# Optimization experiments

Hardware: AMD Instinct MI355X
Metric: run time of the kernel (lower is better)

Reference implementation:

```python
import jax, jax.numpy as jnp
import numpy as np

B, N, S, D, H, ITERS = 32, 4096, 24, 256, 4, 3
DH = D // H
SCALE = DH ** -0.5
EPS = 1e-8
LN_EPS = 1e-5


def _ln(x, g, b):
    m = x.mean(-1, keepdims=True)
    v = ((x - m) ** 2).mean(-1, keepdims=True)
    return (x - m) * jax.lax.rsqrt(v + LN_EPS) * g + b


def setup_inputs() -> dict:
    key = jax.random.key(0)
    ks = jax.random.split(key, 20)
    xav = lambda k, fi, fo: jax.random.uniform(k, (fi, fo), jnp.float32, -1.0, 1.0) * np.sqrt(6.0 / (fi + fo))
    u = lambda k, shp, fan: jax.random.uniform(k, shp, jnp.float32, -1.0, 1.0) / np.sqrt(fan)
    return {
        "extracted_features": jax.random.normal(ks[0], (B, N, D), jnp.float32),
        "conditioning": jax.random.normal(ks[1], (B, S, D), jnp.float32),
        "pos_ln_g": jnp.ones((D,), jnp.float32),
        "pos_ln_b": jnp.zeros((D,), jnp.float32),
        "pos_w1": xav(ks[2], D, D),
        "pos_b1": jnp.zeros((D,), jnp.float32),
        "pos_w2": xav(ks[3], D, D),
        "pos_b2": jnp.zeros((D,), jnp.float32),
        "in_ln_g": jnp.ones((D,), jnp.float32),
        "in_ln_b": jnp.zeros((D,), jnp.float32),
        "slot_ln_g": jnp.ones((D,), jnp.float32),
        "slot_ln_b": jnp.zeros((D,), jnp.float32),
        "Wq": u(ks[4], (D, D), D),
        "Wk": u(ks[5], (D, D), D),
        "Wv": u(ks[6], (D, D), D),
        "gru_wi": u(ks[7], (D, 3 * D), D),  # x @ gru_wi, torch weight_ih.T
        "gru_wh": u(ks[8], (D, 3 * D), D),
        "gru_bi": u(ks[9], (3 * D,), D),
        "gru_bh": u(ks[10], (3 * D,), D),
    }


def reference(extracted_features, conditioning, pos_ln_g, pos_ln_b, pos_w1, pos_b1,
              pos_w2, pos_b2, in_ln_g, in_ln_b, slot_ln_g, slot_ln_b,
              Wq, Wk, Wv, gru_wi, gru_wh, gru_bi, gru_bh):
    b, n, _ = extracted_features.shape
    s = conditioning.shape[1]
    # positional embedding MLP: LN -> Linear -> ReLU -> Linear
    feats = _ln(extracted_features, pos_ln_g, pos_ln_b)
    feats = jax.nn.relu(feats @ pos_w1 + pos_b1) @ pos_w2 + pos_b2
    # slot attention input norm + k/v projections
    inp = _ln(feats, in_ln_g, in_ln_b)
    k = (inp @ Wk).reshape(b, n, H, DH)
    v = (inp @ Wv).reshape(b, n, H, DH)

    slots = conditioning
    attn_before = None
    for _ in range(ITERS):
        slots_prev = slots
        sn = _ln(slots, slot_ln_g, slot_ln_b)
        q = (sn @ Wq).reshape(b, s, H, DH)
        dots = jnp.einsum('bihd,bjhd->bihj', q, k) * SCALE  # [b,s,H,n]
        # softmax over flattened (slot, head) axis per input token
        attn = jax.nn.softmax(dots.reshape(b, s * H, n), axis=1).reshape(b, s, H, n)
        attn_before = attn
        attn_r = (attn + EPS)
        attn_r = attn_r / attn_r.sum(-1, keepdims=True)
        updates = jnp.einsum('bjhd,bihj->bihd', v, attn_r).reshape(b * s, D)
        # GRUCell update
        h = slots_prev.reshape(b * s, D)
        gi = updates @ gru_wi + gru_bi
        gh = h @ gru_wh + gru_bh
        ir, iz, inn = jnp.split(gi, 3, axis=-1)
        hr, hz, hn = jnp.split(gh, 3, axis=-1)
        r = jax.nn.sigmoid(ir + hr)
        z = jax.nn.sigmoid(iz + hz)
        nn_ = jnp.tanh(inn + r * hn)
        slots = ((1.0 - z) * nn_ + z * h).reshape(b, s, D)

    return slots, attn_before.mean(axis=2)
```

## Files before the change

kernel.cpp:

```cpp
#include <hip/hip_runtime.h>
#include <hip/hip_bf16.h>
#include <stdint.h>

typedef __hip_bfloat16 bf16;
typedef __attribute__((ext_vector_type(8))) short short8;
typedef __attribute__((ext_vector_type(4))) float floatx4;

#define DEV __device__ __forceinline__

DEV float bf2f(bf16 v) { return __bfloat162float(v); }
DEV bf16 f2b(float f) { return __float2bfloat16(f); }
DEV unsigned short f2bu(float f) {
  bf16 h = __float2bfloat16(f);
  union { bf16 h; unsigned short u; } c; c.h = h; return c.u;
}


__global__ void detect_kernel(const unsigned short* probe, int* flag) {
  *flag = (probe[0] != 0) ? 1 : 0;
}

__global__ __launch_bounds__(256) void params_kernel(
    const void* s0, const void* s1, const void* s2, const void* s3, const void* s4,
    const void* s5, const void* s6, const void* s7, const void* s8, const void* s9,
    float* dst, const int* flagp)
{
  int idx = blockIdx.x * 256 + threadIdx.x;
  if (idx >= 3584) return;
  const void* srcs[10] = {s0, s1, s2, s3, s4, s5, s6, s7, s8, s9};
  int a, off;
  if (idx < 2048)      { a = idx >> 8; off = idx & 255; }
  else if (idx < 2816) { a = 8; off = idx - 2048; }
  else                 { a = 9; off = idx - 2816; }
  float v = (*flagp) ? bf2f(((const bf16*)srcs[a])[off]) : ((const float*)srcs[a])[off];
  dst[idx] = v;
}

__global__ __launch_bounds__(256) void transpose_convert_kernel(
    const void* src, bf16* dst, int R, int C, const int* flagp)
{
  int idx = blockIdx.x * 256 + threadIdx.x;
  if (idx >= R * C) return;
  int r = idx / C, c = idx - r * C;
  bf16 v = (*flagp) ? ((const bf16*)src)[idx] : f2b(((const float*)src)[idx]);
  dst[(size_t)c * R + r] = v;
}

template<bool OUT_BF16, bool RELU, bool HAS_BIAS>
__global__ __launch_bounds__(256) void gemm_kernel(
    const bf16* __restrict__ A, const bf16* __restrict__ Bt,
    const float* __restrict__ bias, void* __restrict__ C,
    int M, int N, int K)
{
  __shared__ short As[128 * 72];
  __shared__ short Bs[128 * 72];
  const int tid = threadIdx.x;
  const int lane = tid & 63;
  const int wave = tid >> 6;
  const int wr = wave >> 1, wc = wave & 1;
  const int m16 = lane & 15, quad = lane >> 4;
  const long m0 = (long)blockIdx.y * 128, n0 = (long)blockIdx.x * 128;

  floatx4 acc[4][4];
#pragma unroll
  for (int i = 0; i < 4; i++)
#pragma unroll
    for (int j = 0; j < 4; j++) acc[i][j] = {0.f, 0.f, 0.f, 0.f};

  const int srow = tid >> 3;
  const int scol = (tid & 7) * 8;

  for (int kb = 0; kb < K; kb += 64) {
#pragma unroll
    for (int p = 0; p < 4; p++) {
      int row = srow + p * 32;
      uint4 av = *(const uint4*)(A + (m0 + row) * (long)K + kb + scol);
      *(uint4*)(&As[row * 72 + scol]) = av;
      uint4 bv = *(const uint4*)(Bt + (n0 + row) * (long)K + kb + scol);
      *(uint4*)(&Bs[row * 72 + scol]) = bv;
    }
    __syncthreads();
#pragma unroll
    for (int ks = 0; ks < 2; ks++) {
      short8 af[4], bfr[4];
#pragma unroll
      for (int t = 0; t < 4; t++) {
        af[t]  = *(const short8*)(&As[(wr * 64 + t * 16 + m16) * 72 + ks * 32 + quad * 8]);
        bfr[t] = *(const short8*)(&Bs[(wc * 64 + t * 16 + m16) * 72 + ks * 32 + quad * 8]);
      }
#pragma unroll
      for (int mt = 0; mt < 4; mt++)
#pragma unroll
        for (int nt = 0; nt < 4; nt++)
          acc[mt][nt] = __builtin_amdgcn_mfma_f32_16x16x32_bf16(af[mt], bfr[nt], acc[mt][nt], 0, 0, 0);
    }
    __syncthreads();
  }

#pragma unroll
  for (int mt = 0; mt < 4; mt++) {
#pragma unroll
    for (int nt = 0; nt < 4; nt++) {
      long col = n0 + wc * 64 + nt * 16 + m16;
      float bb = HAS_BIAS ? bias[col] : 0.f;
#pragma unroll
      for (int r = 0; r < 4; r++) {
        long row = m0 + wr * 64 + mt * 16 + quad * 4 + r;
        float v = acc[mt][nt][r] + bb;
        if (RELU) v = fmaxf(v, 0.f);
        if (OUT_BF16) ((bf16*)C)[row * N + col] = f2b(v);
        else          ((float*)C)[row * N + col] = v;
      }
    }
  }
}

template<int MODE>
__global__ __launch_bounds__(256) void ln_kernel(
    const void* __restrict__ xin, const float* __restrict__ g, const float* __restrict__ bb,
    bf16* __restrict__ out, int rows, const int* flagp)
{
  int wave = threadIdx.x >> 6, lane = threadIdx.x & 63;
  long row = (long)blockIdx.x * 4 + wave;
  if (row >= rows) return;
  float v[4];
  bool f32in = (MODE == 1) || (MODE == 2 && *flagp == 0);
  if (f32in) {
    float4 f = *(const float4*)((const float*)xin + row * 256 + lane * 4);
    v[0] = f.x; v[1] = f.y; v[2] = f.z; v[3] = f.w;
  } else {
    uint2 u = *(const uint2*)((const bf16*)xin + row * 256 + lane * 4);
    v[0] = __uint_as_float((u.x & 0xffffu) << 16);
    v[1] = __uint_as_float(u.x & 0xffff0000u);
    v[2] = __uint_as_float((u.y & 0xffffu) << 16);
    v[3] = __uint_as_float(u.y & 0xffff0000u);
  }
  float s = v[0] + v[1] + v[2] + v[3];
  float sq = v[0] * v[0] + v[1] * v[1] + v[2] * v[2] + v[3] * v[3];
#pragma unroll
  for (int off = 32; off > 0; off >>= 1) {
    s  += __shfl_xor(s, off);
    sq += __shfl_xor(sq, off);
  }
  float m = s * (1.f / 256.f);
  float var = sq * (1.f / 256.f) - m * m;
  float rs = rsqrtf(var + 1e-5f);
  float4 gv = *(const float4*)(g + lane * 4);
  float4 bv = *(const float4*)(bb + lane * 4);
  union { unsigned short us[4]; uint2 u; } pk;
  pk.us[0] = f2bu((v[0] - m) * rs * gv.x + bv.x);
  pk.us[1] = f2bu((v[1] - m) * rs * gv.y + bv.y);
  pk.us[2] = f2bu((v[2] - m) * rs * gv.z + bv.z);
  pk.us[3] = f2bu((v[3] - m) * rs * gv.w + bv.w);
  *(uint2*)(out + row * 256 + lane * 4) = pk.u;
}

__global__ __launch_bounds__(256) void init_slots_kernel(
    const void* __restrict__ cond, float* __restrict__ sF, bf16* __restrict__ sB,
    const int* flagp)
{
  int idx = blockIdx.x * 256 + threadIdx.x;
  float v = (*flagp) ? bf2f(((const bf16*)cond)[idx]) : ((const float*)cond)[idx];
  sF[idx] = v;
  sB[idx] = f2b(v);
}

__global__ __launch_bounds__(256) void repack_q_kernel(
    const float* __restrict__ q, bf16* __restrict__ qp)
{
  int idx = blockIdx.x * 256 + threadIdx.x;
  int dh = idx & 63, m = (idx >> 6) & 31, h = (idx >> 11) & 3, b = idx >> 13;
  float val = 0.f;
  if (m < 24) val = q[((size_t)(b * 24 + m)) * 256 + h * 64 + dh] * 0.125f;
  qp[idx] = f2b(val);
}

template<bool LAST>
__global__ __launch_bounds__(256) void attn_iter_kernel(
    const bf16* __restrict__ qp, const bf16* __restrict__ kbuf,
    const bf16* __restrict__ vT, float* __restrict__ pupd,
    void* __restrict__ out, const int* flagp)
{
  const int js = blockIdx.x;
  const int b  = blockIdx.y;
  const int h  = threadIdx.x >> 6;
  const int lane = threadIdx.x & 63;
  const int m16 = lane & 15, quad = lane >> 4;
  const int j0 = js * 128;

  __shared__ unsigned short att[4 * 24 * 136];
  __shared__ float red1[4 * 132];
  __shared__ float red2[4 * 132];

  short8 qf[2][2];
  const bf16* qpb = qp + (size_t)(b * 4 + h) * 2048;
#pragma unroll
  for (int mt = 0; mt < 2; mt++)
#pragma unroll
    for (int ks = 0; ks < 2; ks++)
      qf[mt][ks] = *(const short8*)(qpb + (mt * 16 + m16) * 64 + ks * 32 + quad * 8);

  floatx4 dacc[2][8];
#pragma unroll
  for (int i = 0; i < 2; i++)
#pragma unroll
    for (int j = 0; j < 8; j++) dacc[i][j] = {0.f, 0.f, 0.f, 0.f};

  const bf16* kb = kbuf + ((size_t)b * 4096 + j0) * 256 + h * 64;
#pragma unroll
  for (int ks = 0; ks < 2; ks++)
#pragma unroll
    for (int nt = 0; nt < 8; nt++) {
      short8 bfr = *(const short8*)(kb + (size_t)(nt * 16 + m16) * 256 + ks * 32 + quad * 8);
      dacc[0][nt] = __builtin_amdgcn_mfma_f32_16x16x32_bf16(qf[0][ks], bfr, dacc[0][nt], 0, 0, 0);
      dacc[1][nt] = __builtin_amdgcn_mfma_f32_16x16x32_bf16(qf[1][ks], bfr, dacc[1][nt], 0, 0, 0);
    }

  const bool mt1_valid = (quad < 2);

  float cmax[8];
#pragma unroll
  for (int nt = 0; nt < 8; nt++) {
    float m = fmaxf(fmaxf(dacc[0][nt][0], dacc[0][nt][1]), fmaxf(dacc[0][nt][2], dacc[0][nt][3]));
    if (mt1_valid)
      m = fmaxf(m, fmaxf(fmaxf(dacc[1][nt][0], dacc[1][nt][1]), fmaxf(dacc[1][nt][2], dacc[1][nt][3])));
    m = fmaxf(m, __shfl_xor(m, 16));
    m = fmaxf(m, __shfl_xor(m, 32));
    cmax[nt] = m;
  }
  if (quad == 0) {
#pragma unroll
    for (int nt = 0; nt < 8; nt++) red1[h * 132 + nt * 16 + m16] = cmax[nt];
  }
  __syncthreads();

  float csum[8];
#pragma unroll
  for (int nt = 0; nt < 8; nt++) {
    int c = nt * 16 + m16;
    float g = fmaxf(fmaxf(red1[c], red1[132 + c]), fmaxf(red1[264 + c], red1[396 + c]));
    float s = 0.f;
#pragma unroll
    for (int r = 0; r < 4; r++) {
      float e = __expf(dacc[0][nt][r] - g);
      dacc[0][nt][r] = e; s += e;
    }
#pragma unroll
    for (int r = 0; r < 4; r++) {
      float e = mt1_valid ? __expf(dacc[1][nt][r] - g) : 0.f;
      dacc[1][nt][r] = e; s += e;
    }
    s += __shfl_xor(s, 16);
    s += __shfl_xor(s, 32);
    csum[nt] = s;
  }
  if (quad == 0) {
#pragma unroll
    for (int nt = 0; nt < 8; nt++) red2[h * 132 + nt * 16 + m16] = csum[nt];
  }
  __syncthreads();

  float wsum[2][4] = {{0.f, 0.f, 0.f, 0.f}, {0.f, 0.f, 0.f, 0.f}};
#pragma unroll
  for (int nt = 0; nt < 8; nt++) {
    int c = nt * 16 + m16;
    float inv = 1.f / (red2[c] + red2[132 + c] + red2[264 + c] + red2[396 + c]);
#pragma unroll
    for (int r = 0; r < 4; r++) {
      float a = dacc[0][nt][r] * inv + 1e-8f;
      int row = quad * 4 + r;
      att[h * 3264 + row * 136 + c] = f2bu(a);
      wsum[0][r] += a;
    }
    if (mt1_valid) {
#pragma unroll
      for (int r = 0; r < 4; r++) {
        float a = dacc[1][nt][r] * inv + 1e-8f;
        int row = 16 + quad * 4 + r;
        att[h * 3264 + row * 136 + c] = f2bu(a);
        wsum[1][r] += a;
      }
    }
  }
#pragma unroll
  for (int mt = 0; mt < 2; mt++)
#pragma unroll
    for (int r = 0; r < 4; r++) {
      float w = wsum[mt][r];
      w += __shfl_xor(w, 1); w += __shfl_xor(w, 2);
      w += __shfl_xor(w, 4); w += __shfl_xor(w, 8);
      wsum[mt][r] = w;
    }
  float* dst = pupd + ((size_t)(b * 4 + h) * 32 + js) * 1920;
  if (m16 == 0) {
#pragma unroll
    for (int mt = 0; mt < 2; mt++)
#pragma unroll
      for (int r = 0; r < 4; r++) {
        int row = mt * 16 + quad * 4 + r;
        if (row < 24) dst[row * 80 + 64] = wsum[mt][r];
      }
  }
  __syncthreads();

  floatx4 uacc[2][4];
#pragma unroll
  for (int i = 0; i < 2; i++)
#pragma unroll
    for (int j = 0; j < 4; j++) uacc[i][j] = {0.f, 0.f, 0.f, 0.f};
  int arow1 = 16 + m16; if (arow1 > 23) arow1 = 23;
  const bf16* vb0 = vT + (size_t)b * 4096 + j0;
#pragma unroll
  for (int ks = 0; ks < 4; ks++) {
    short8 a0 = *(const short8*)(&att[h * 3264 + m16 * 136 + ks * 32 + quad * 8]);
    short8 a1 = *(const short8*)(&att[h * 3264 + arow1 * 136 + ks * 32 + quad * 8]);
#pragma unroll
    for (int nt = 0; nt < 4; nt++) {
      short8 bfr = *(const short8*)(vb0 + (size_t)(h * 64 + nt * 16 + m16) * 131072 + ks * 32 + quad * 8);
      uacc[0][nt] = __builtin_amdgcn_mfma_f32_16x16x32_bf16(a0, bfr, uacc[0][nt], 0, 0, 0);
      uacc[1][nt] = __builtin_amdgcn_mfma_f32_16x16x32_bf16(a1, bfr, uacc[1][nt], 0, 0, 0);
    }
  }
#pragma unroll
  for (int mt = 0; mt < 2; mt++)
#pragma unroll
    for (int nt = 0; nt < 4; nt++)
#pragma unroll
      for (int r = 0; r < 4; r++) {
        int row = mt * 16 + quad * 4 + r;
        if (row < 24) dst[row * 80 + nt * 16 + m16] = uacc[mt][nt][r];
      }

  if (LAST) {
    int c = threadIdx.x & 127;
    int half = threadIdx.x >> 7;
#pragma unroll
    for (int i0 = 0; i0 < 12; i0++) {
      int i = half * 12 + i0;
      float s = bf2f(__ushort_as_bfloat16(att[i * 136 + c]))
              + bf2f(__ushort_as_bfloat16(att[3264 + i * 136 + c]))
              + bf2f(__ushort_as_bfloat16(att[6528 + i * 136 + c]))
              + bf2f(__ushort_as_bfloat16(att[9792 + i * 136 + c]));
      size_t oidx = ((size_t)(b * 24 + i)) * 4096 + j0 + c;
      if (*flagp) ((bf16*)out)[196608 + oidx] = f2b(0.25f * s);
      else        ((float*)out)[196608 + oidx] = 0.25f * s;
    }
  }
}

__global__ __launch_bounds__(256) void upd_final_kernel(
    const float* __restrict__ pupd, bf16* __restrict__ updB)
{
  int bh = blockIdx.x; int b = bh >> 2, h = bh & 3;
  int idx = blockIdx.y * 256 + threadIdx.x;
  int i = idx >> 6, d = idx & 63;
  const float* base = pupd + (size_t)bh * 32 * 1920 + i * 80;
  float v = 0.f, w = 0.f;
#pragma unroll
  for (int p = 0; p < 32; p++) {
    v += base[p * 1920 + d];
    w += base[p * 1920 + 64];
  }
  updB[((size_t)(b * 24 + i)) * 256 + h * 64 + d] = f2b(v / w);
}

__global__ __launch_bounds__(256) void gru_gate_kernel(
    const float* __restrict__ gi, const float* __restrict__ gh,
    float* __restrict__ sF, bf16* __restrict__ sB)
{
  int row = blockIdx.x, d = threadIdx.x;
  size_t o = (size_t)row * 768;
  float ir = gi[o + d], iz = gi[o + 256 + d], inn = gi[o + 512 + d];
  float hr = gh[o + d], hz = gh[o + 256 + d], hn = gh[o + 512 + d];
  float hv = sF[(size_t)row * 256 + d];
  float r = 1.f / (1.f + __expf(-(ir + hr)));
  float z = 1.f / (1.f + __expf(-(iz + hz)));
  float nn = tanhf(inn + r * hn);
  float sv = (1.f - z) * nn + z * hv;
  sF[(size_t)row * 256 + d] = sv;
  sB[(size_t)row * 256 + d] = f2b(sv);
}

__global__ __launch_bounds__(256) void out_slots_kernel(
    const float* __restrict__ sF, void* __restrict__ out, const int* flagp)
{
  int idx = blockIdx.x * 256 + threadIdx.x;
  float v = sF[idx];
  if (*flagp) ((bf16*)out)[idx] = f2b(v);
  else        ((float*)out)[idx] = v;
}

static constexpr size_t SZ_BIG   = (size_t)32 * 4096 * 256 * 2;
static constexpr size_t OFF_BUF1 = 0;
static constexpr size_t OFF_BUF2 = OFF_BUF1 + SZ_BIG;
static constexpr size_t OFF_K    = OFF_BUF2 + SZ_BIG;
static constexpr size_t OFF_V    = OFF_K + SZ_BIG;
static constexpr size_t OFF_Q    = OFF_V + SZ_BIG;
static constexpr size_t OFF_QP   = OFF_Q + (size_t)768 * 256 * 4;
static constexpr size_t OFF_SNB  = OFF_QP + (size_t)32 * 4 * 32 * 64 * 2;
static constexpr size_t OFF_SF   = OFF_SNB + (size_t)768 * 256 * 2;
static constexpr size_t OFF_SB   = OFF_SF + (size_t)768 * 256 * 4;
static constexpr size_t OFF_UPD  = OFF_SB + (size_t)768 * 256 * 2;
static constexpr size_t OFF_GI   = OFF_UPD + (size_t)768 * 256 * 2;
static constexpr size_t OFF_GH   = OFF_GI + (size_t)768 * 768 * 4;
static constexpr size_t OFF_PUPD = OFF_GH + (size_t)768 * 768 * 4;
static constexpr size_t OFF_W1T  = OFF_PUPD + (size_t)128 * 32 * 1920 * 4;
static constexpr size_t OFF_W2T  = OFF_W1T + (size_t)256 * 256 * 2;
static constexpr size_t OFF_WQT  = OFF_W2T + (size_t)256 * 256 * 2;
static constexpr size_t OFF_WKT  = OFF_WQT + (size_t)256 * 256 * 2;
static constexpr size_t OFF_WVT  = OFF_WKT + (size_t)256 * 256 * 2;
static constexpr size_t OFF_GWIT = OFF_WVT + (size_t)256 * 256 * 2;
static constexpr size_t OFF_GWHT = OFF_GWIT + (size_t)256 * 768 * 2;
static constexpr size_t OFF_PAR  = OFF_GWHT + (size_t)256 * 768 * 2;
static constexpr size_t OFF_FLAG = OFF_PAR + (size_t)3584 * 4;
static constexpr size_t WS_NEED  = OFF_FLAG + 256;

extern "C" void kernel_launch(void* const* d_in, const int* in_sizes, int n_in,
                              void* d_out, int out_size, void* d_ws, size_t ws_size,
                              hipStream_t stream) {
  (void)in_sizes; (void)n_in; (void)out_size;
  if (ws_size < WS_NEED) return;

  const void* x         = d_in[0];
  const void* cond      = d_in[1];
  const void* pos_ln_g  = d_in[2];
  const void* pos_ln_b  = d_in[3];
  const void* pos_w1    = d_in[4];
  const void* pos_b1    = d_in[5];
  const void* pos_w2    = d_in[6];
  const void* pos_b2    = d_in[7];
  const void* in_ln_g   = d_in[8];
  const void* in_ln_b   = d_in[9];
  const void* slot_ln_g = d_in[10];
  const void* slot_ln_b = d_in[11];
  const void* Wq        = d_in[12];
  const void* Wk        = d_in[13];
  const void* Wv        = d_in[14];
  const void* gru_wi    = d_in[15];
  const void* gru_wh    = d_in[16];
  const void* gru_bi    = d_in[17];
  const void* gru_bh    = d_in[18];

  char* ws = (char*)d_ws;
  bf16*  buf1  = (bf16*)(ws + OFF_BUF1);
  bf16*  buf2  = (bf16*)(ws + OFF_BUF2);
  bf16*  kbuf  = (bf16*)(ws + OFF_K);
  bf16*  vT    = (bf16*)(ws + OFF_V);
  float* qbuf  = (float*)(ws + OFF_Q);
  bf16*  qp    = (bf16*)(ws + OFF_QP);
  bf16*  snb   = (bf16*)(ws + OFF_SNB);
  float* sF    = (float*)(ws + OFF_SF);
  bf16*  sB    = (bf16*)(ws + OFF_SB);
  bf16*  updB  = (bf16*)(ws + OFF_UPD);
  float* gi    = (float*)(ws + OFF_GI);
  float* gh    = (float*)(ws + OFF_GH);
  float* pupd  = (float*)(ws + OFF_PUPD);
  bf16*  w1t   = (bf16*)(ws + OFF_W1T);
  bf16*  w2t   = (bf16*)(ws + OFF_W2T);
  bf16*  wqt   = (bf16*)(ws + OFF_WQT);
  bf16*  wkt   = (bf16*)(ws + OFF_WKT);
  bf16*  wvt   = (bf16*)(ws + OFF_WVT);
  bf16*  gwit  = (bf16*)(ws + OFF_GWIT);
  bf16*  gwht  = (bf16*)(ws + OFF_GWHT);
  float* par   = (float*)(ws + OFF_PAR);
  int*   flagp = (int*)(ws + OFF_FLAG);

  detect_kernel<<<1, 1, 0, stream>>>((const unsigned short*)pos_ln_g, flagp);
  params_kernel<<<14, 256, 0, stream>>>(pos_ln_g, pos_ln_b, pos_b1, pos_b2,
                                        in_ln_g, in_ln_b, slot_ln_g, slot_ln_b,
                                        gru_bi, gru_bh, par, flagp);
  transpose_convert_kernel<<<256, 256, 0, stream>>>(pos_w1, w1t, 256, 256, flagp);
  transpose_convert_kernel<<<256, 256, 0, stream>>>(pos_w2, w2t, 256, 256, flagp);
  transpose_convert_kernel<<<256, 256, 0, stream>>>(Wq, wqt, 256, 256, flagp);
  transpose_convert_kernel<<<256, 256, 0, stream>>>(Wk, wkt, 256, 256, flagp);
  transpose_convert_kernel<<<256, 256, 0, stream>>>(Wv, wvt, 256, 256, flagp);
  transpose_convert_kernel<<<768, 256, 0, stream>>>(gru_wi, gwit, 256, 768, flagp);
  transpose_convert_kernel<<<768, 256, 0, stream>>>(gru_wh, gwht, 256, 768, flagp);
  init_slots_kernel<<<768, 256, 0, stream>>>(cond, sF, sB, flagp);

  ln_kernel<2><<<32768, 256, 0, stream>>>(x, par + 0, par + 256, buf1, 131072, flagp);
  gemm_kernel<true, true, true><<<dim3(2, 1024), 256, 0, stream>>>(
      buf1, w1t, par + 512, buf2, 131072, 256, 256);
  gemm_kernel<true, false, true><<<dim3(2, 1024), 256, 0, stream>>>(
      buf2, w2t, par + 768, buf1, 131072, 256, 256);
  ln_kernel<0><<<32768, 256, 0, stream>>>(buf1, par + 1024, par + 1280, buf2, 131072, flagp);
  gemm_kernel<true, false, false><<<dim3(2, 1024), 256, 0, stream>>>(
      buf2, wkt, nullptr, kbuf, 131072, 256, 256);
  gemm_kernel<true, false, false><<<dim3(1024, 2), 256, 0, stream>>>(
      wvt, buf2, nullptr, vT, 256, 131072, 256);

  for (int it = 0; it < 3; it++) {
    ln_kernel<1><<<192, 256, 0, stream>>>(sF, par + 1536, par + 1792, snb, 768, flagp);
    gemm_kernel<false, false, false><<<dim3(2, 6), 256, 0, stream>>>(
        snb, wqt, nullptr, qbuf, 768, 256, 256);
    repack_q_kernel<<<1024, 256, 0, stream>>>(qbuf, qp);
    if (it == 2)
      attn_iter_kernel<true><<<dim3(32, 32), 256, 0, stream>>>(qp, kbuf, vT, pupd, d_out, flagp);
    else
      attn_iter_kernel<false><<<dim3(32, 32), 256, 0, stream>>>(qp, kbuf, vT, pupd, d_out, flagp);
    upd_final_kernel<<<dim3(128, 6), 256, 0, stream>>>(pupd, updB);
    gemm_kernel<false, false, true><<<dim3(6, 6), 256, 0, stream>>>(
        updB, gwit, par + 2048, gi, 768, 768, 256);
    gemm_kernel<false, false, true><<<dim3(6, 6), 256, 0, stream>>>(
        sB, gwht, par + 2816, gh, 768, 768, 256);
    gru_gate_kernel<<<768, 256, 0, stream>>>(gi, gh, sF, sB);
  }

  out_slots_kernel<<<768, 256, 0, stream>>>(sF, d_out, flagp);
}
```

Measured before the change: 679.8 us.

## Fuse layernorms into GEMMs, merge weight prep and GRU GEMMs, widen attention tiles

```diff
diff --git a/kernel.cpp b/kernel.cpp
--- a/kernel.cpp
+++ b/kernel.cpp
@@ -14,52 +14,72 @@
   bf16 h = __float2bfloat16(f);
   union { bf16 h; unsigned short u; } c; c.h = h; return c.u;
 }
-
-
-__global__ void detect_kernel(const unsigned short* probe, int* flag) {
-  *flag = (probe[0] != 0) ? 1 : 0;
-}
+DEV bool is_bf16_in(const void* probe) { return ((const unsigned short*)probe)[0] != 0; }
+
 
 __global__ __launch_bounds__(256) void params_kernel(
     const void* s0, const void* s1, const void* s2, const void* s3, const void* s4,
     const void* s5, const void* s6, const void* s7, const void* s8, const void* s9,
-    float* dst, const int* flagp)
+    float* dst)
 {
   int idx = blockIdx.x * 256 + threadIdx.x;
   if (idx >= 3584) return;
+  bool bf = is_bf16_in(s0);
   const void* srcs[10] = {s0, s1, s2, s3, s4, s5, s6, s7, s8, s9};
   int a, off;
   if (idx < 2048)      { a = idx >> 8; off = idx & 255; }
   else if (idx < 2816) { a = 8; off = idx - 2048; }
   else                 { a = 9; off = idx - 2816; }
-  float v = (*flagp) ? bf2f(((const bf16*)srcs[a])[off]) : ((const float*)srcs[a])[off];
+  float v = bf ? bf2f(((const bf16*)srcs[a])[off]) : ((const float*)srcs[a])[off];
   dst[idx] = v;
 }
 
-__global__ __launch_bounds__(256) void transpose_convert_kernel(
-    const void* src, bf16* dst, int R, int C, const int* flagp)
+__global__ __launch_bounds__(256) void transpose_all_kernel(
+    const void* w1, const void* w2, const void* wq, const void* wk, const void* wv,
+    const void* gwi, const void* gwh,
+    bf16* d1, bf16* d2, bf16* dq, bf16* dk, bf16* dv, bf16* dgi, bf16* dgh,
+    const void* probe)
 {
   int idx = blockIdx.x * 256 + threadIdx.x;
-  if (idx >= R * C) return;
-  int r = idx / C, c = idx - r * C;
-  bf16 v = (*flagp) ? ((const bf16*)src)[idx] : f2b(((const float*)src)[idx]);
-  dst[(size_t)c * R + r] = v;
+  if (idx >= 720896) return;
+  bool bf = is_bf16_in(probe);
+  const void* src; bf16* dst; int C, off;
+  if (idx < 327680) {
+    int wsel = idx >> 16; off = idx & 65535; C = 256;
+    const void* S[5] = {w1, w2, wq, wk, wv};
+    bf16* D[5] = {d1, d2, dq, dk, dv};
+    src = S[wsel]; dst = D[wsel];
+  } else {
+    int j = idx - 327680; int wsel = j / 196608; off = j - wsel * 196608; C = 768;
+    src = wsel ? gwh : gwi; dst = wsel ? dgh : dgi;
+  }
+  int r = off / C, c = off - r * C;
+  bf16 v = bf ? ((const bf16*)src)[off] : f2b(((const float*)src)[off]);
+  dst[(size_t)c * 256 + r] = v;
+}
+
+__global__ __launch_bounds__(256) void init_slots_kernel(
+    const void* __restrict__ cond, float* __restrict__ sF, bf16* __restrict__ sB,
+    const void* probe)
+{
+  int idx = blockIdx.x * 256 + threadIdx.x;
+  bool bf = is_bf16_in(probe);
+  float v = bf ? bf2f(((const bf16*)cond)[idx]) : ((const float*)cond)[idx];
+  sF[idx] = v;
+  sB[idx] = f2b(v);
 }
 
 template<bool OUT_BF16, bool RELU, bool HAS_BIAS>
-__global__ __launch_bounds__(256) void gemm_kernel(
-    const bf16* __restrict__ A, const bf16* __restrict__ Bt,
-    const float* __restrict__ bias, void* __restrict__ C,
-    int M, int N, int K)
-{
-  __shared__ short As[128 * 72];
-  __shared__ short Bs[128 * 72];
+DEV void gemm_body(const bf16* __restrict__ A, const bf16* __restrict__ Bt,
+                   const float* __restrict__ bias, void* __restrict__ C,
+                   int M, int N, int K, int bx, int by, short* As, short* Bs)
+{
   const int tid = threadIdx.x;
   const int lane = tid & 63;
   const int wave = tid >> 6;
   const int wr = wave >> 1, wc = wave & 1;
   const int m16 = lane & 15, quad = lane >> 4;
-  const long m0 = (long)blockIdx.y * 128, n0 = (long)blockIdx.x * 128;
+  const long m0 = (long)by * 128, n0 = (long)bx * 128;
 
   floatx4 acc[4][4];
 #pragma unroll
@@ -115,78 +135,290 @@
   }
 }
 
-template<int MODE>
-__global__ __launch_bounds__(256) void ln_kernel(
-    const void* __restrict__ xin, const float* __restrict__ g, const float* __restrict__ bb,
-    bf16* __restrict__ out, int rows, const int* flagp)
-{
-  int wave = threadIdx.x >> 6, lane = threadIdx.x & 63;
-  long row = (long)blockIdx.x * 4 + wave;
-  if (row >= rows) return;
-  float v[4];
-  bool f32in = (MODE == 1) || (MODE == 2 && *flagp == 0);
-  if (f32in) {
-    float4 f = *(const float4*)((const float*)xin + row * 256 + lane * 4);
-    v[0] = f.x; v[1] = f.y; v[2] = f.z; v[3] = f.w;
-  } else {
-    uint2 u = *(const uint2*)((const bf16*)xin + row * 256 + lane * 4);
+template<bool OUT_BF16, bool RELU, bool HAS_BIAS>
+__global__ __launch_bounds__(256) void gemm_kernel(
+    const bf16* __restrict__ A, const bf16* __restrict__ Bt,
+    const float* __restrict__ bias, void* __restrict__ C,
+    int M, int N, int K)
+{
+  __shared__ short As[128 * 72];
+  __shared__ short Bs[128 * 72];
+  gemm_body<OUT_BF16, RELU, HAS_BIAS>(A, Bt, bias, C, M, N, K, blockIdx.x, blockIdx.y, As, Bs);
+}
+
+__global__ __launch_bounds__(256) void gru2_kernel(
+    const bf16* __restrict__ updB, const bf16* __restrict__ sB,
+    const bf16* __restrict__ gwit, const bf16* __restrict__ gwht,
+    const float* __restrict__ par, float* __restrict__ gi, float* __restrict__ gh)
+{
+  __shared__ short As[128 * 72];
+  __shared__ short Bs[128 * 72];
+  if (blockIdx.z == 0)
+    gemm_body<false, false, true>(updB, gwit, par + 2048, gi, 768, 768, 256,
+                                  blockIdx.x, blockIdx.y, As, Bs);
+  else
+    gemm_body<false, false, true>(sB, gwht, par + 2816, gh, 768, 768, 256,
+                                  blockIdx.x, blockIdx.y, As, Bs);
+}
+
+__global__ __launch_bounds__(512) void g1ln_kernel(
+    const void* __restrict__ x, const bf16* __restrict__ w1t,
+    const float* __restrict__ par, bf16* __restrict__ h1, const void* probe)
+{
+  __shared__ short As[128 * 256];
+  const int tid = threadIdx.x;
+  const int lane = tid & 63;
+  const int wave = tid >> 6;
+  const int wr = wave >> 2, wc = wave & 3;
+  const int m16 = lane & 15, quad = lane >> 4;
+  const long m0 = (long)blockIdx.x * 128;
+  const bool bfin = is_bf16_in(probe);
+
+  float4 gv = *(const float4*)(par + lane * 4);
+  float4 bv = *(const float4*)(par + 256 + lane * 4);
+#pragma unroll
+  for (int i = 0; i < 16; i++) {
+    int row = wave * 16 + i;
+    float v[4];
+    if (bfin) {
+      uint2 u = *(const uint2*)((const bf16*)x + (m0 + row) * 256 + lane * 4);
+      v[0] = __uint_as_float((u.x & 0xffffu) << 16);
+      v[1] = __uint_as_float(u.x & 0xffff0000u);
+      v[2] = __uint_as_float((u.y & 0xffffu) << 16);
+      v[3] = __uint_as_float(u.y & 0xffff0000u);
+    } else {
+      float4 f = *(const float4*)((const float*)x + (m0 + row) * 256 + lane * 4);
+      v[0] = f.x; v[1] = f.y; v[2] = f.z; v[3] = f.w;
+    }
+    float s = v[0] + v[1] + v[2] + v[3];
+    float sq = v[0] * v[0] + v[1] * v[1] + v[2] * v[2] + v[3] * v[3];
+#pragma unroll
+    for (int off = 32; off > 0; off >>= 1) { s += __shfl_xor(s, off); sq += __shfl_xor(sq, off); }
+    float mn = s * (1.f / 256.f);
+    float rs = rsqrtf(sq * (1.f / 256.f) - mn * mn + 1e-5f);
+    union { unsigned short us[4]; uint2 u; } pk;
+    pk.us[0] = f2bu((v[0] - mn) * rs * gv.x + bv.x);
+    pk.us[1] = f2bu((v[1] - mn) * rs * gv.y + bv.y);
+    pk.us[2] = f2bu((v[2] - mn) * rs * gv.z + bv.z);
+    pk.us[3] = f2bu((v[3] - mn) * rs * gv.w + bv.w);
+    *(uint2*)(&As[row * 256 + ((lane * 4) ^ ((row & 7) << 3))]) = pk.u;
+  }
+  __syncthreads();
+
+  floatx4 acc[4][4];
+#pragma unroll
+  for (int i = 0; i < 4; i++)
+#pragma unroll
+    for (int j = 0; j < 4; j++) acc[i][j] = {0.f, 0.f, 0.f, 0.f};
+
+#pragma unroll
+  for (int ks = 0; ks < 8; ks++) {
+    short8 af[4], bfr[4];
+#pragma unroll
+    for (int t = 0; t < 4; t++) {
+      int row = wr * 64 + t * 16 + m16;
+      af[t] = *(const short8*)(&As[row * 256 + ((ks * 32 + quad * 8) ^ ((row & 7) << 3))]);
+      bfr[t] = *(const short8*)(w1t + (size_t)(wc * 64 + t * 16 + m16) * 256 + ks * 32 + quad * 8);
+    }
+#pragma unroll
+    for (int mt = 0; mt < 4; mt++)
+#pragma unroll
+      for (int nt = 0; nt < 4; nt++)
+        acc[mt][nt] = __builtin_amdgcn_mfma_f32_16x16x32_bf16(af[mt], bfr[nt], acc[mt][nt], 0, 0, 0);
+  }
+
+#pragma unroll
+  for (int mt = 0; mt < 4; mt++)
+#pragma unroll
+    for (int nt = 0; nt < 4; nt++) {
+      int col = wc * 64 + nt * 16 + m16;
+      float bb = par[512 + col];
+#pragma unroll
+      for (int r = 0; r < 4; r++) {
+        long row = m0 + wr * 64 + mt * 16 + quad * 4 + r;
+        h1[row * 256 + col] = f2b(fmaxf(acc[mt][nt][r] + bb, 0.f));
+      }
+    }
+}
+
+__global__ __launch_bounds__(512) void kvln_kernel(
+    const bf16* __restrict__ feats, const bf16* __restrict__ wkt, const bf16* __restrict__ wvt,
+    const float* __restrict__ par, bf16* __restrict__ kbuf, bf16* __restrict__ vT)
+{
+  __shared__ short As[128 * 256];
+  const int tid = threadIdx.x;
+  const int lane = tid & 63;
+  const int wave = tid >> 6;
+  const int wr = wave >> 2, wc = wave & 3;
+  const int m16 = lane & 15, quad = lane >> 4;
+  const long m0 = (long)blockIdx.x * 128;
+
+#pragma unroll
+  for (int i = 0; i < 8; i++) {
+    int idx = tid + i * 512;
+    int row = idx >> 5, col = (idx & 31) * 8;
+    short8 vls = *(const short8*)(feats + (m0 + row) * 256 + col);
+    *(short8*)(&As[row * 256 + (col ^ ((row & 7) << 3))]) = vls;
+  }
+  __syncthreads();
+
+  float4 gv = *(const float4*)(par + 1024 + lane * 4);
+  float4 bv = *(const float4*)(par + 1280 + lane * 4);
+#pragma unroll
+  for (int i = 0; i < 16; i++) {
+    int row = wave * 16 + i;
+    int ci = (lane * 4) ^ ((row & 7) << 3);
+    uint2 u = *(const uint2*)(&As[row * 256 + ci]);
+    float v[4];
     v[0] = __uint_as_float((u.x & 0xffffu) << 16);
     v[1] = __uint_as_float(u.x & 0xffff0000u);
     v[2] = __uint_as_float((u.y & 0xffffu) << 16);
     v[3] = __uint_as_float(u.y & 0xffff0000u);
-  }
-  float s = v[0] + v[1] + v[2] + v[3];
-  float sq = v[0] * v[0] + v[1] * v[1] + v[2] * v[2] + v[3] * v[3];
-#pragma unroll
-  for (int off = 32; off > 0; off >>= 1) {
-    s  += __shfl_xor(s, off);
-    sq += __shfl_xor(sq, off);
-  }
-  float m = s * (1.f / 256.f);
-  float var = sq * (1.f / 256.f) - m * m;
-  float rs = rsqrtf(var + 1e-5f);
-  float4 gv = *(const float4*)(g + lane * 4);
-  float4 bv = *(const float4*)(bb + lane * 4);
-  union { unsigned short us[4]; uint2 u; } pk;
-  pk.us[0] = f2bu((v[0] - m) * rs * gv.x + bv.x);
-  pk.us[1] = f2bu((v[1] - m) * rs * gv.y + bv.y);
-  pk.us[2] = f2bu((v[2] - m) * rs * gv.z + bv.z);
-  pk.us[3] = f2bu((v[3] - m) * rs * gv.w + bv.w);
-  *(uint2*)(out + row * 256 + lane * 4) = pk.u;
-}
-
-__global__ __launch_bounds__(256) void init_slots_kernel(
-    const void* __restrict__ cond, float* __restrict__ sF, bf16* __restrict__ sB,
-    const int* flagp)
-{
-  int idx = blockIdx.x * 256 + threadIdx.x;
-  float v = (*flagp) ? bf2f(((const bf16*)cond)[idx]) : ((const float*)cond)[idx];
-  sF[idx] = v;
-  sB[idx] = f2b(v);
-}
-
-__global__ __launch_bounds__(256) void repack_q_kernel(
-    const float* __restrict__ q, bf16* __restrict__ qp)
-{
-  int idx = blockIdx.x * 256 + threadIdx.x;
-  int dh = idx & 63, m = (idx >> 6) & 31, h = (idx >> 11) & 3, b = idx >> 13;
-  float val = 0.f;
-  if (m < 24) val = q[((size_t)(b * 24 + m)) * 256 + h * 64 + dh] * 0.125f;
-  qp[idx] = f2b(val);
+    float s = v[0] + v[1] + v[2] + v[3];
+    float sq = v[0] * v[0] + v[1] * v[1] + v[2] * v[2] + v[3] * v[3];
+#pragma unroll
+    for (int off = 32; off > 0; off >>= 1) { s += __shfl_xor(s, off); sq += __shfl_xor(sq, off); }
+    float mn = s * (1.f / 256.f);
+    float rs = rsqrtf(sq * (1.f / 256.f) - mn * mn + 1e-5f);
+    union { unsigned short us[4]; uint2 u; } pk;
+    pk.us[0] = f2bu((v[0] - mn) * rs * gv.x + bv.x);
+    pk.us[1] = f2bu((v[1] - mn) * rs * gv.y + bv.y);
+    pk.us[2] = f2bu((v[2] - mn) * rs * gv.z + bv.z);
+    pk.us[3] = f2bu((v[3] - mn) * rs * gv.w + bv.w);
+    *(uint2*)(&As[row * 256 + ci]) = pk.u;
+  }
+  __syncthreads();
+
+#pragma unroll
+  for (int proj = 0; proj < 2; proj++) {
+    const bf16* W = proj ? wvt : wkt;
+    floatx4 acc[4][4];
+#pragma unroll
+    for (int i = 0; i < 4; i++)
+#pragma unroll
+      for (int j = 0; j < 4; j++) acc[i][j] = {0.f, 0.f, 0.f, 0.f};
+#pragma unroll
+    for (int ks = 0; ks < 8; ks++) {
+      short8 af[4], bfr[4];
+#pragma unroll
+      for (int t = 0; t < 4; t++) {
+        int row = wr * 64 + t * 16 + m16;
+        af[t] = *(const short8*)(&As[row * 256 + ((ks * 32 + quad * 8) ^ ((row & 7) << 3))]);
+        bfr[t] = *(const short8*)(W + (size_t)(wc * 64 + t * 16 + m16) * 256 + ks * 32 + quad * 8);
+      }
+#pragma unroll
+      for (int mt = 0; mt < 4; mt++)
+#pragma unroll
+        for (int nt = 0; nt < 4; nt++)
+          acc[mt][nt] = __builtin_amdgcn_mfma_f32_16x16x32_bf16(af[mt], bfr[nt], acc[mt][nt], 0, 0, 0);
+    }
+    if (proj == 0) {
+#pragma unroll
+      for (int mt = 0; mt < 4; mt++)
+#pragma unroll
+        for (int nt = 0; nt < 4; nt++) {
+          int col = wc * 64 + nt * 16 + m16;
+#pragma unroll
+          for (int r = 0; r < 4; r++) {
+            long row = m0 + wr * 64 + mt * 16 + quad * 4 + r;
+            kbuf[row * 256 + col] = f2b(acc[mt][nt][r]);
+          }
+        }
+    } else {
+#pragma unroll
+      for (int mt = 0; mt < 4; mt++)
+#pragma unroll
+        for (int nt = 0; nt < 4; nt++) {
+          int d = wc * 64 + nt * 16 + m16;
+          long t0 = m0 + wr * 64 + mt * 16 + quad * 4;
+          union { unsigned short us[4]; uint2 u; } pk;
+#pragma unroll
+          for (int r = 0; r < 4; r++) pk.us[r] = f2bu(acc[mt][nt][r]);
+          *(uint2*)(vT + (size_t)d * 131072 + t0) = pk.u;
+        }
+    }
+  }
+}
+
+__global__ __launch_bounds__(256) void lnq_kernel(
+    const float* __restrict__ sF, const bf16* __restrict__ wqt,
+    const float* __restrict__ par, bf16* __restrict__ qp)
+{
+  __shared__ short As[32 * 264];
+  const int tid = threadIdx.x;
+  const int lane = tid & 63;
+  const int wave = tid >> 6;
+  const int m16 = lane & 15, quad = lane >> 4;
+  const int b = blockIdx.x;
+
+  for (int i = tid; i < 8 * 264; i += 256) As[24 * 264 + i] = 0;
+
+  float4 gv = *(const float4*)(par + 1536 + lane * 4);
+  float4 bv = *(const float4*)(par + 1792 + lane * 4);
+#pragma unroll
+  for (int i = 0; i < 6; i++) {
+    int row = wave * 6 + i;
+    float4 f = *(const float4*)(sF + ((size_t)(b * 24 + row)) * 256 + lane * 4);
+    float v[4] = {f.x, f.y, f.z, f.w};
+    float s = v[0] + v[1] + v[2] + v[3];
+    float sq = v[0] * v[0] + v[1] * v[1] + v[2] * v[2] + v[3] * v[3];
+#pragma unroll
+    for (int off = 32; off > 0; off >>= 1) { s += __shfl_xor(s, off); sq += __shfl_xor(sq, off); }
+    float mn = s * (1.f / 256.f);
+    float rs = rsqrtf(sq * (1.f / 256.f) - mn * mn + 1e-5f);
+    union { unsigned short us[4]; uint2 u; } pk;
+    pk.us[0] = f2bu((v[0] - mn) * rs * gv.x + bv.x);
+    pk.us[1] = f2bu((v[1] - mn) * rs * gv.y + bv.y);
+    pk.us[2] = f2bu((v[2] - mn) * rs * gv.z + bv.z);
+    pk.us[3] = f2bu((v[3] - mn) * rs * gv.w + bv.w);
+    *(uint2*)(&As[row * 264 + lane * 4]) = pk.u;
+  }
+  __syncthreads();
+
+  floatx4 acc[2][4];
+#pragma unroll
+  for (int i = 0; i < 2; i++)
+#pragma unroll
+    for (int j = 0; j < 4; j++) acc[i][j] = {0.f, 0.f, 0.f, 0.f};
+#pragma unroll
+  for (int ks = 0; ks < 8; ks++) {
+    short8 af[2], bfr[4];
+#pragma unroll
+    for (int mt = 0; mt < 2; mt++)
+      af[mt] = *(const short8*)(&As[(mt * 16 + m16) * 264 + ks * 32 + quad * 8]);
+#pragma unroll
+    for (int nt = 0; nt < 4; nt++)
+      bfr[nt] = *(const short8*)(wqt + (size_t)(wave * 64 + nt * 16 + m16) * 256 + ks * 32 + quad * 8);
+#pragma unroll
+    for (int mt = 0; mt < 2; mt++)
+#pragma unroll
+      for (int nt = 0; nt < 4; nt++)
+        acc[mt][nt] = __builtin_amdgcn_mfma_f32_16x16x32_bf16(af[mt], bfr[nt], acc[mt][nt], 0, 0, 0);
+  }
+
+  bf16* qpb = qp + (size_t)(b * 4 + wave) * 2048;
+#pragma unroll
+  for (int mt = 0; mt < 2; mt++)
+#pragma unroll
+    for (int nt = 0; nt < 4; nt++)
+#pragma unroll
+      for (int r = 0; r < 4; r++) {
+        int m = mt * 16 + quad * 4 + r;
+        qpb[m * 64 + nt * 16 + m16] = f2b(acc[mt][nt][r] * 0.125f);
+      }
 }
 
 template<bool LAST>
 __global__ __launch_bounds__(256) void attn_iter_kernel(
     const bf16* __restrict__ qp, const bf16* __restrict__ kbuf,
     const bf16* __restrict__ vT, float* __restrict__ pupd,
-    void* __restrict__ out, const int* flagp)
+    void* __restrict__ out, const void* __restrict__ probe)
 {
   const int js = blockIdx.x;
   const int b  = blockIdx.y;
   const int h  = threadIdx.x >> 6;
   const int lane = threadIdx.x & 63;
   const int m16 = lane & 15, quad = lane >> 4;
-  const int j0 = js * 128;
 
   __shared__ unsigned short att[4 * 24 * 136];
   __shared__ float red1[4 * 132];
@@ -200,88 +432,131 @@
     for (int ks = 0; ks < 2; ks++)
       qf[mt][ks] = *(const short8*)(qpb + (mt * 16 + m16) * 64 + ks * 32 + quad * 8);
 
-  floatx4 dacc[2][8];
+  const bool mt1_valid = (quad < 2);
+  int arow1 = 16 + m16; if (arow1 > 23) arow1 = 23;
+
+  floatx4 uacc[2][4];
 #pragma unroll
   for (int i = 0; i < 2; i++)
 #pragma unroll
-    for (int j = 0; j < 8; j++) dacc[i][j] = {0.f, 0.f, 0.f, 0.f};
-
-  const bf16* kb = kbuf + ((size_t)b * 4096 + j0) * 256 + h * 64;
-#pragma unroll
-  for (int ks = 0; ks < 2; ks++)
+    for (int j = 0; j < 4; j++) uacc[i][j] = {0.f, 0.f, 0.f, 0.f};
+  float wsum[2][4] = {{0.f, 0.f, 0.f, 0.f}, {0.f, 0.f, 0.f, 0.f}};
+
+  for (int hh = 0; hh < 2; hh++) {
+    const int j0 = js * 256 + hh * 128;
+
+    floatx4 dacc[2][8];
+#pragma unroll
+    for (int i = 0; i < 2; i++)
+#pragma unroll
+      for (int j = 0; j < 8; j++) dacc[i][j] = {0.f, 0.f, 0.f, 0.f};
+
+    const bf16* kb = kbuf + ((size_t)b * 4096 + j0) * 256 + h * 64;
+#pragma unroll
+    for (int ks = 0; ks < 2; ks++)
+#pragma unroll
+      for (int nt = 0; nt < 8; nt++) {
+        short8 bfr = *(const short8*)(kb + (size_t)(nt * 16 + m16) * 256 + ks * 32 + quad * 8);
+        dacc[0][nt] = __builtin_amdgcn_mfma_f32_16x16x32_bf16(qf[0][ks], bfr, dacc[0][nt], 0, 0, 0);
+        dacc[1][nt] = __builtin_amdgcn_mfma_f32_16x16x32_bf16(qf[1][ks], bfr, dacc[1][nt], 0, 0, 0);
+      }
+
+    float cmax[8];
 #pragma unroll
     for (int nt = 0; nt < 8; nt++) {
-      short8 bfr = *(const short8*)(kb + (size_t)(nt * 16 + m16) * 256 + ks * 32 + quad * 8);
-      dacc[0][nt] = __builtin_amdgcn_mfma_f32_16x16x32_bf16(qf[0][ks], bfr, dacc[0][nt], 0, 0, 0);
-      dacc[1][nt] = __builtin_amdgcn_mfma_f32_16x16x32_bf16(qf[1][ks], bfr, dacc[1][nt], 0, 0, 0);
-    }
-
-  const bool mt1_valid = (quad < 2);
-
-  float cmax[8];
-#pragma unroll
-  for (int nt = 0; nt < 8; nt++) {
-    float m = fmaxf(fmaxf(dacc[0][nt][0], dacc[0][nt][1]), fmaxf(dacc[0][nt][2], dacc[0][nt][3]));
-    if (mt1_valid)
-      m = fmaxf(m, fmaxf(fmaxf(dacc[1][nt][0], dacc[1][nt][1]), fmaxf(dacc[1][nt][2], dacc[1][nt][3])));
-    m = fmaxf(m, __shfl_xor(m, 16));
-    m = fmaxf(m, __shfl_xor(m, 32));
-    cmax[nt] = m;
-  }
-  if (quad == 0) {
-#pragma unroll
-    for (int nt = 0; nt < 8; nt++) red1[h * 132 + nt * 16 + m16] = cmax[nt];
-  }
-  __syncthreads();
-
-  float csum[8];
-#pragma unroll
-  for (int nt = 0; nt < 8; nt++) {
-    int c = nt * 16 + m16;
-    float g = fmaxf(fmaxf(red1[c], red1[132 + c]), fmaxf(red1[264 + c], red1[396 + c]));
-    float s = 0.f;
-#pragma unroll
-    for (int r = 0; r < 4; r++) {
-      float e = __expf(dacc[0][nt][r] - g);
-      dacc[0][nt][r] = e; s += e;
-    }
-#pragma unroll
-    for (int r = 0; r < 4; r++) {
-      float e = mt1_valid ? __expf(dacc[1][nt][r] - g) : 0.f;
-      dacc[1][nt][r] = e; s += e;
-    }
-    s += __shfl_xor(s, 16);
-    s += __shfl_xor(s, 32);
-    csum[nt] = s;
-  }
-  if (quad == 0) {
-#pragma unroll
-    for (int nt = 0; nt < 8; nt++) red2[h * 132 + nt * 16 + m16] = csum[nt];
-  }
-  __syncthreads();
-
-  float wsum[2][4] = {{0.f, 0.f, 0.f, 0.f}, {0.f, 0.f, 0.f, 0.f}};
-#pragma unroll
-  for (int nt = 0; nt < 8; nt++) {
-    int c = nt * 16 + m16;
-    float inv = 1.f / (red2[c] + red2[132 + c] + red2[264 + c] + red2[396 + c]);
-#pragma unroll
-    for (int r = 0; r < 4; r++) {
-      float a = dacc[0][nt][r] * inv + 1e-8f;
-      int row = quad * 4 + r;
-      att[h * 3264 + row * 136 + c] = f2bu(a);
-      wsum[0][r] += a;
-    }
-    if (mt1_valid) {
+      float m = fmaxf(fmaxf(dacc[0][nt][0], dacc[0][nt][1]), fmaxf(dacc[0][nt][2], dacc[0][nt][3]));
+      if (mt1_valid)
+        m = fmaxf(m, fmaxf(fmaxf(dacc[1][nt][0], dacc[1][nt][1]), fmaxf(dacc[1][nt][2], dacc[1][nt][3])));
+      m = fmaxf(m, __shfl_xor(m, 16));
+      m = fmaxf(m, __shfl_xor(m, 32));
+      cmax[nt] = m;
+    }
+    if (quad == 0) {
+#pragma unroll
+      for (int nt = 0; nt < 8; nt++) red1[h * 132 + nt * 16 + m16] = cmax[nt];
+    }
+    __syncthreads();
+
+    float csum[8];
+#pragma unroll
+    for (int nt = 0; nt < 8; nt++) {
+      int c = nt * 16 + m16;
+      float g = fmaxf(fmaxf(red1[c], red1[132 + c]), fmaxf(red1[264 + c], red1[396 + c]));
+      float s = 0.f;
 #pragma unroll
       for (int r = 0; r < 4; r++) {
-        float a = dacc[1][nt][r] * inv + 1e-8f;
-        int row = 16 + quad * 4 + r;
-        att[h * 3264 + row * 136 + c] = f2bu(a);
-        wsum[1][r] += a;
-      }
-    }
-  }
+        float e = __expf(dacc[0][nt][r] - g);
+        dacc[0][nt][r] = e; s += e;
+      }
+#pragma unroll
+      for (int r = 0; r < 4; r++) {
+        float e = mt1_valid ? __expf(dacc[1][nt][r] - g) : 0.f;
+        dacc[1][nt][r] = e; s += e;
+      }
+      s += __shfl_xor(s, 16);
+      s += __shfl_xor(s, 32);
+      csum[nt] = s;
+    }
+    if (quad == 0) {
+#pragma unroll
+      for (int nt = 0; nt < 8; nt++) red2[h * 132 + nt * 16 + m16] = csum[nt];
+    }
+    __syncthreads();
+
+#pragma unroll
+    for (int nt = 0; nt < 8; nt++) {
+      int c = nt * 16 + m16;
+      float inv = 1.f / (red2[c] + red2[132 + c] + red2[264 + c] + red2[396 + c]);
+#pragma unroll
+      for (int r = 0; r < 4; r++) {
+        float a = dacc[0][nt][r] * inv + 1e-8f;
+        att[h * 3264 + (quad * 4 + r) * 136 + c] = f2bu(a);
+        wsum[0][r] += a;
+      }
+      if (mt1_valid) {
+#pragma unroll
+        for (int r = 0; r < 4; r++) {
+          float a = dacc[1][nt][r] * inv + 1e-8f;
+          att[h * 3264 + (16 + quad * 4 + r) * 136 + c] = f2bu(a);
+          wsum[1][r] += a;
+        }
+      }
+    }
+    __syncthreads();
+
+    const bf16* vb0 = vT + (size_t)b * 4096 + j0;
+#pragma unroll
+    for (int ks = 0; ks < 4; ks++) {
+      short8 a0 = *(const short8*)(&att[h * 3264 + m16 * 136 + ks * 32 + quad * 8]);
+      short8 a1 = *(const short8*)(&att[h * 3264 + arow1 * 136 + ks * 32 + quad * 8]);
+#pragma unroll
+      for (int nt = 0; nt < 4; nt++) {
+        short8 bfr = *(const short8*)(vb0 + (size_t)(h * 64 + nt * 16 + m16) * 131072 + ks * 32 + quad * 8);
+        uacc[0][nt] = __builtin_amdgcn_mfma_f32_16x16x32_bf16(a0, bfr, uacc[0][nt], 0, 0, 0);
+        uacc[1][nt] = __builtin_amdgcn_mfma_f32_16x16x32_bf16(a1, bfr, uacc[1][nt], 0, 0, 0);
+      }
+    }
+
+    if (LAST) {
+      const bool bfo = is_bf16_in(probe);
+      int c = threadIdx.x & 127;
+      int half = threadIdx.x >> 7;
+#pragma unroll
+      for (int i0 = 0; i0 < 12; i0++) {
+        int i = half * 12 + i0;
+        float s = bf2f(__ushort_as_bfloat16(att[i * 136 + c]))
+                + bf2f(__ushort_as_bfloat16(att[3264 + i * 136 + c]))
+                + bf2f(__ushort_as_bfloat16(att[6528 + i * 136 + c]))
+                + bf2f(__ushort_as_bfloat16(att[9792 + i * 136 + c]));
+        size_t oidx = ((size_t)(b * 24 + i)) * 4096 + j0 + c;
+        if (bfo) ((bf16*)out)[196608 + oidx] = f2b(0.25f * s);
+        else     ((float*)out)[196608 + oidx] = 0.25f * s;
+      }
+    }
+    __syncthreads();
+  }
+
+  float* dst = pupd + ((size_t)((b * 4 + h) * 16 + js)) * 1920;
 #pragma unroll
   for (int mt = 0; mt < 2; mt++)
 #pragma unroll
@@ -291,7 +566,6 @@
       w += __shfl_xor(w, 4); w += __shfl_xor(w, 8);
       wsum[mt][r] = w;
     }
-  float* dst = pupd + ((size_t)(b * 4 + h) * 32 + js) * 1920;
   if (m16 == 0) {
 #pragma unroll
     for (int mt = 0; mt < 2; mt++)
@@ -301,26 +575,6 @@
         if (row < 24) dst[row * 80 + 64] = wsum[mt][r];
       }
   }
-  __syncthreads();
-
-  floatx4 uacc[2][4];
-#pragma unroll
-  for (int i = 0; i < 2; i++)
-#pragma unroll
-    for (int j = 0; j < 4; j++) uacc[i][j] = {0.f, 0.f, 0.f, 0.f};
-  int arow1 = 16 + m16; if (arow1 > 23) arow1 = 23;
-  const bf16* vb0 = vT + (size_t)b * 4096 + j0;
-#pragma unroll
-  for (int ks = 0; ks < 4; ks++) {
-    short8 a0 = *(const short8*)(&att[h * 3264 + m16 * 136 + ks * 32 + quad * 8]);
-    short8 a1 = *(const short8*)(&att[h * 3264 + arow1 * 136 + ks * 32 + quad * 8]);
-#pragma unroll
-    for (int nt = 0; nt < 4; nt++) {
-      short8 bfr = *(const short8*)(vb0 + (size_t)(h * 64 + nt * 16 + m16) * 131072 + ks * 32 + quad * 8);
-      uacc[0][nt] = __builtin_amdgcn_mfma_f32_16x16x32_bf16(a0, bfr, uacc[0][nt], 0, 0, 0);
-      uacc[1][nt] = __builtin_amdgcn_mfma_f32_16x16x32_bf16(a1, bfr, uacc[1][nt], 0, 0, 0);
-    }
-  }
 #pragma unroll
   for (int mt = 0; mt < 2; mt++)
 #pragma unroll
@@ -330,22 +584,6 @@
         int row = mt * 16 + quad * 4 + r;
         if (row < 24) dst[row * 80 + nt * 16 + m16] = uacc[mt][nt][r];
       }
-
-  if (LAST) {
-    int c = threadIdx.x & 127;
-    int half = threadIdx.x >> 7;
-#pragma unroll
-    for (int i0 = 0; i0 < 12; i0++) {
-      int i = half * 12 + i0;
-      float s = bf2f(__ushort_as_bfloat16(att[i * 136 + c]))
-              + bf2f(__ushort_as_bfloat16(att[3264 + i * 136 + c]))
-              + bf2f(__ushort_as_bfloat16(att[6528 + i * 136 + c]))
-              + bf2f(__ushort_as_bfloat16(att[9792 + i * 136 + c]));
-      size_t oidx = ((size_t)(b * 24 + i)) * 4096 + j0 + c;
-      if (*flagp) ((bf16*)out)[196608 + oidx] = f2b(0.25f * s);
-      else        ((float*)out)[196608 + oidx] = 0.25f * s;
-    }
-  }
 }
 
 __global__ __launch_bounds__(256) void upd_final_kernel(
@@ -354,19 +592,21 @@
   int bh = blockIdx.x; int b = bh >> 2, h = bh & 3;
   int idx = blockIdx.y * 256 + threadIdx.x;
   int i = idx >> 6, d = idx & 63;
-  const float* base = pupd + (size_t)bh * 32 * 1920 + i * 80;
+  const float* base = pupd + (size_t)bh * 16 * 1920 + i * 80;
   float v = 0.f, w = 0.f;
 #pragma unroll
-  for (int p = 0; p < 32; p++) {
+  for (int p = 0; p < 16; p++) {
     v += base[p * 1920 + d];
     w += base[p * 1920 + 64];
   }
   updB[((size_t)(b * 24 + i)) * 256 + h * 64 + d] = f2b(v / w);
 }
 
+template<bool LAST>
 __global__ __launch_bounds__(256) void gru_gate_kernel(
     const float* __restrict__ gi, const float* __restrict__ gh,
-    float* __restrict__ sF, bf16* __restrict__ sB)
+    float* __restrict__ sF, bf16* __restrict__ sB,
+    void* __restrict__ out, const void* __restrict__ probe)
 {
   int row = blockIdx.x, d = threadIdx.x;
   size_t o = (size_t)row * 768;
@@ -379,15 +619,10 @@
   float sv = (1.f - z) * nn + z * hv;
   sF[(size_t)row * 256 + d] = sv;
   sB[(size_t)row * 256 + d] = f2b(sv);
-}
-
-__global__ __launch_bounds__(256) void out_slots_kernel(
-    const float* __restrict__ sF, void* __restrict__ out, const int* flagp)
-{
-  int idx = blockIdx.x * 256 + threadIdx.x;
-  float v = sF[idx];
-  if (*flagp) ((bf16*)out)[idx] = f2b(v);
-  else        ((float*)out)[idx] = v;
+  if (LAST) {
+    if (is_bf16_in(probe)) ((bf16*)out)[(size_t)row * 256 + d] = f2b(sv);
+    else                   ((float*)out)[(size_t)row * 256 + d] = sv;
+  }
 }
 
 static constexpr size_t SZ_BIG   = (size_t)32 * 4096 * 256 * 2;
@@ -446,9 +681,7 @@
   bf16*  buf2  = (bf16*)(ws + OFF_BUF2);
   bf16*  kbuf  = (bf16*)(ws + OFF_K);
   bf16*  vT    = (bf16*)(ws + OFF_V);
-  float* qbuf  = (float*)(ws + OFF_Q);
   bf16*  qp    = (bf16*)(ws + OFF_QP);
-  bf16*  snb   = (bf16*)(ws + OFF_SNB);
   float* sF    = (float*)(ws + OFF_SF);
   bf16*  sB    = (bf16*)(ws + OFF_SB);
   bf16*  updB  = (bf16*)(ws + OFF_UPD);
@@ -463,48 +696,32 @@
   bf16*  gwit  = (bf16*)(ws + OFF_GWIT);
   bf16*  gwht  = (bf16*)(ws + OFF_GWHT);
   float* par   = (float*)(ws + OFF_PAR);
-  int*   flagp = (int*)(ws + OFF_FLAG);
-
-  detect_kernel<<<1, 1, 0, stream>>>((const unsigned short*)pos_ln_g, flagp);
+
+  const void* probe = pos_ln_g;
+
   params_kernel<<<14, 256, 0, stream>>>(pos_ln_g, pos_ln_b, pos_b1, pos_b2,
                                         in_ln_g, in_ln_b, slot_ln_g, slot_ln_b,
-                                        gru_bi, gru_bh, par, flagp);
-  transpose_convert_kernel<<<256, 256, 0, stream>>>(pos_w1, w1t, 256, 256, flagp);
-  transpose_convert_kernel<<<256, 256, 0, stream>>>(pos_w2, w2t, 256, 256, flagp);
-  transpose_convert_kernel<<<256, 256, 0, stream>>>(Wq, wqt, 256, 256, flagp);
-  transpose_convert_kernel<<<256, 256, 0, stream>>>(Wk, wkt, 256, 256, flagp);
-  transpose_convert_kernel<<<256, 256, 0, stream>>>(Wv, wvt, 256, 256, flagp);
-  transpose_convert_kernel<<<768, 256, 0, stream>>>(gru_wi, gwit, 256, 768, flagp);
-  transpose_convert_kernel<<<768, 256, 0, stream>>>(gru_wh, gwht, 256, 768, flagp);
-  init_slots_kernel<<<768, 256, 0, stream>>>(cond, sF, sB, flagp);
-
-  ln_kernel<2><<<32768, 256, 0, stream>>>(x, par + 0, par + 256, buf1, 131072, flagp);
-  gemm_kernel<true, true, true><<<dim3(2, 1024), 256, 0, stream>>>(
-      buf1, w1t, par + 512, buf2, 131072, 256, 256);
+                                        gru_bi, gru_bh, par);
+  transpose_all_kernel<<<2816, 256, 0, stream>>>(pos_w1, pos_w2, Wq, Wk, Wv, gru_wi, gru_wh,
+                                                 w1t, w2t, wqt, wkt, wvt, gwit, gwht, probe);
+  init_slots_kernel<<<768, 256, 0, stream>>>(cond, sF, sB, probe);
+
+  g1ln_kernel<<<1024, 512, 0, stream>>>(x, w1t, par, buf1, probe);
   gemm_kernel<true, false, true><<<dim3(2, 1024), 256, 0, stream>>>(
-      buf2, w2t, par + 768, buf1, 131072, 256, 256);
-  ln_kernel<0><<<32768, 256, 0, stream>>>(buf1, par + 1024, par + 1280, buf2, 131072, flagp);
-  gemm_kernel<true, false, false><<<dim3(2, 1024), 256, 0, stream>>>(
-      buf2, wkt, nullptr, kbuf, 131072, 256, 256);
-  gemm_kernel<true, false, false><<<dim3(1024, 2), 256, 0, stream>>>(
-      wvt, buf2, nullptr, vT, 256, 131072, 256);
+      buf1, w2t, par + 768, buf2, 131072, 256, 256);
+  kvln_kernel<<<1024, 512, 0, stream>>>(buf2, wkt, wvt, par, kbuf, vT);
 
   for (int it = 0; it < 3; it++) {
-    ln_kernel<1><<<192, 256, 0, stream>>>(sF, par + 1536, par + 1792, snb, 768, flagp);
-    gemm_kernel<false, false, false><<<dim3(2, 6), 256, 0, stream>>>(
-        snb, wqt, nullptr, qbuf, 768, 256, 256);
-    repack_q_kernel<<<1024, 256, 0, stream>>>(qbuf, qp);
+    lnq_kernel<<<32, 256, 0, stream>>>(sF, wqt, par, qp);
     if (it == 2)
-      attn_iter_kernel<true><<<dim3(32, 32), 256, 0, stream>>>(qp, kbuf, vT, pupd, d_out, flagp);
+      attn_iter_kernel<true><<<dim3(16, 32), 256, 0, stream>>>(qp, kbuf, vT, pupd, d_out, probe);
     else
-      attn_iter_kernel<false><<<dim3(32, 32), 256, 0, stream>>>(qp, kbuf, vT, pupd, d_out, flagp);
+      attn_iter_kernel<false><<<dim3(16, 32), 256, 0, stream>>>(qp, kbuf, vT, pupd, d_out, probe);
     upd_final_kernel<<<dim3(128, 6), 256, 0, stream>>>(pupd, updB);
-    gemm_kernel<false, false, true><<<dim3(6, 6), 256, 0, stream>>>(
-        updB, gwit, par + 2048, gi, 768, 768, 256);
-    gemm_kernel<false, false, true><<<dim3(6, 6), 256, 0, stream>>>(
-        sB, gwht, par + 2816, gh, 768, 768, 256);
-    gru_gate_kernel<<<768, 256, 0, stream>>>(gi, gh, sF, sB);
-  }
-
-  out_slots_kernel<<<768, 256, 0, stream>>>(sF, d_out, flagp);
-}
+    gru2_kernel<<<dim3(6, 6, 2), 256, 0, stream>>>(updB, sB, gwit, gwht, par, gi, gh);
+    if (it == 2)
+      gru_gate_kernel<true><<<768, 256, 0, stream>>>(gi, gh, sF, sB, d_out, probe);
+    else
+      gru_gate_kernel<false><<<768, 256, 0, stream>>>(gi, gh, sF, sB, d_out, probe);
+  }
+}
```

Result: faster. 651.1 us (-4.2%).
